# Kernel optimization log

Hardware: AMD Instinct MI355X
Metric: run time of the kernel (lower is better)

The kernel has to match this reference:

```python
import jax, jax.numpy as jnp
import numpy as np

B, L, D, C, H, NB = 2, 2048, 256, 8, 8, 2
S = 2                        # spatial coord dim of s
E = 2 * D - (C + 1)          # id-embedding width per D*2-(C+1)
FIN = 1 + S + E + C          # z + s + id-embed + conditionals
MAXLOC = 4096
DH = (2 * D) // H            # per-head dim


def _ln(x, sc, b):
    m = x.mean(-1, keepdims=True)
    v = ((x - m) ** 2).mean(-1, keepdims=True)
    return (x - m) * jax.lax.rsqrt(v + 1e-6) * sc + b


def setup_inputs() -> dict:
    key = jax.random.key(0)
    ks = iter(jax.random.split(key, 64))
    nrm = lambda shape: jax.random.normal(next(ks), shape, jnp.float32) * 0.02
    inp = {
        "z": jax.random.normal(next(ks), (B, L), jnp.float32),
        "conditionals": jax.random.normal(next(ks), (C,), jnp.float32),
        "s": jax.random.uniform(next(ks), (L, S), jnp.float32),
        "K": jax.random.uniform(next(ks), (L, L), jnp.float32),
        "embed": nrm((MAXLOC, E)),
        "W_in1": nrm((FIN, 4 * D)), "b_in1": jnp.zeros((4 * D,), jnp.float32),
        "W_in2": nrm((4 * D, D)), "b_in2": jnp.zeros((D,), jnp.float32),
        "bias_w": jnp.ones((NB,), jnp.float32), "bias_b": jnp.zeros((NB,), jnp.float32),
        "Wq": nrm((NB, D, 2 * D)), "bq": jnp.zeros((NB, 2 * D), jnp.float32),
        "Wk": nrm((NB, D, 2 * D)), "bk": jnp.zeros((NB, 2 * D), jnp.float32),
        "Wv": nrm((NB, D, 2 * D)), "bv": jnp.zeros((NB, 2 * D), jnp.float32),
        "Wo": nrm((NB, 2 * D, D)), "bo": jnp.zeros((NB, D), jnp.float32),
        "ln1_s": jnp.ones((NB, D), jnp.float32), "ln1_b": jnp.zeros((NB, D), jnp.float32),
        "ln2_s": jnp.ones((NB, D), jnp.float32), "ln2_b": jnp.zeros((NB, D), jnp.float32),
        "Wf1": nrm((NB, D, 4 * D)), "bf1": jnp.zeros((NB, 4 * D), jnp.float32),
        "Wf2": nrm((NB, 4 * D, D)), "bf2": jnp.zeros((NB, D), jnp.float32),
        "Wh1": nrm((D, 128)), "bh1": jnp.zeros((128,), jnp.float32),
        "Wh2": nrm((128, 1)), "bh2": jnp.zeros((1,), jnp.float32),
    }
    return inp


def reference(z, conditionals, s, K, embed, W_in1, b_in1, W_in2, b_in2,
              bias_w, bias_b, Wq, bq, Wk, bk, Wv, bv, Wo, bo,
              ln1_s, ln1_b, ln2_s, ln2_b, Wf1, bf1, Wf2, bf2,
              Wh1, bh1, Wh2, bh2):
    Bx, Lx = z.shape
    ids_e = embed[:Lx]  # ids = arange(L), so embedding lookup is a leading slice
    feats = jnp.concatenate([
        z[..., None],                                          # (B, L, 1)
        jnp.broadcast_to(s[None], (Bx, Lx, S)),                # (B, L, S)
        jnp.broadcast_to(ids_e[None], (Bx, Lx, E)),            # (B, L, E)
        jnp.broadcast_to(conditionals[None, None], (Bx, Lx, C)),  # cond_as_feats
    ], axis=-1)
    x = jax.nn.gelu(feats @ W_in1 + b_in1) @ W_in2 + b_in2     # (B, L, D)
    for i in range(NB):
        bias = bias_w[i] * K + bias_b[i]                        # learned scalar-affine kernel bias (L, L)
        h = _ln(x, ln1_s[i], ln1_b[i])
        q = (h @ Wq[i] + bq[i]).reshape(Bx, Lx, H, DH)
        k = (h @ Wk[i] + bk[i]).reshape(Bx, Lx, H, DH)
        v = (h @ Wv[i] + bv[i]).reshape(Bx, Lx, H, DH)
        scores = jnp.einsum('bqhd,bkhd->bhqk', q, k) / jnp.sqrt(jnp.float32(DH))
        scores = scores + bias[None, None]                      # broadcast over batch, heads
        a = jax.nn.softmax(scores, axis=-1)
        o = jnp.einsum('bhqk,bkhd->bqhd', a, v).reshape(Bx, Lx, 2 * D)
        x = x + (o @ Wo[i] + bo[i])
        h2 = _ln(x, ln2_s[i], ln2_b[i])
        x = x + jax.nn.gelu(h2 @ Wf1[i] + bf1[i]) @ Wf2[i] + bf2[i]
    return jax.nn.gelu(x @ Wh1 + bh1) @ Wh2 + bh2              # head MLP([128,1]) -> (B, L, 1)
```

## Files before the change

### kernel.cpp

```cpp
#include <hip/hip_runtime.h>
#include <math.h>

#define B_SZ 2
#define L_LEN 2048
#define D_MOD 256
#define H_HEADS 8
#define NB_BLK 2
#define S_SZ 2
#define E_SZ 503
#define C_SZ 8
#define FIN 514
#define FIN_PAD 576
#define LOG2E 1.44269504088896340736f
#define QSC (0.125f * LOG2E)

typedef short bf16x8 __attribute__((ext_vector_type(8)));
typedef float f32x4 __attribute__((ext_vector_type(4)));
typedef unsigned short u16x4 __attribute__((ext_vector_type(4)));
typedef unsigned short u16x8 __attribute__((ext_vector_type(8)));

#define OFF_IN1 0
#define OFF_IN2 589824
#define OFF_QKV 851968
#define OFF_O   1638400
#define OFF_F1  1900544
#define OFF_F2  2424832
#define OFF_H   2949120
#define WT_END  3047424

__device__ __forceinline__ unsigned short f2bf(float x) {
    unsigned u = __float_as_uint(x);
    u += 0x7FFFu + ((u >> 16) & 1u);
    return (unsigned short)(u >> 16);
}

__device__ __forceinline__ float bf2f(unsigned short h) {
    return __uint_as_float(((unsigned)h) << 16);
}

__device__ __forceinline__ float gelu_f(float x) {
    float x3 = x * x * x;
    return 0.5f * x * (1.0f + tanhf(0.7978845608028654f * (x + 0.044715f * x3)));
}

__device__ __forceinline__ void gll16(const void* g, void* l) {
    __builtin_amdgcn_global_load_lds(
        (const __attribute__((address_space(1))) unsigned int*)g,
        (__attribute__((address_space(3))) unsigned int*)l,
        16, 0, 0);
}

__global__ __launch_bounds__(256) void prep_kernel(
    const float* __restrict__ W_in1, const float* __restrict__ W_in2,
    const float* __restrict__ Wq, const float* __restrict__ Wk,
    const float* __restrict__ Wv, const float* __restrict__ Wo,
    const float* __restrict__ Wf1, const float* __restrict__ Wf2,
    const float* __restrict__ Wh1, const float* __restrict__ Kmat,
    const float* __restrict__ bias_w,
    const float* __restrict__ bq, const float* __restrict__ bk,
    const float* __restrict__ bv,
    const float* __restrict__ z, const float* __restrict__ s,
    const float* __restrict__ embed, const float* __restrict__ cond,
    unsigned short* __restrict__ wt, unsigned short* __restrict__ kmfrag,
    float* __restrict__ bqkv, unsigned short* __restrict__ feats)
{
    __shared__ unsigned short sT[64][65];
    int b = blockIdx.x;
    int t = threadIdx.x;

    if (b < 720) {
        const float* src; unsigned short* dst; int K, N, Kp, tile;
        float scale = 1.0f;
        if (b < 144)      { src = W_in1; dst = wt + OFF_IN1; K = 514;  N = 1024; Kp = 576;  tile = b; }
        else if (b < 208) { src = W_in2; dst = wt + OFF_IN2; K = 1024; N = 256;  Kp = 1024; tile = b - 144; }
        else if (b < 400) { int t2 = b - 208;
                            int sec = t2 >> 5; tile = t2 & 31;
                            int i = sec / 3, which = sec % 3;
                            const float* wsrc = which == 0 ? Wq : which == 1 ? Wk : Wv;
                            if (which == 0) scale = QSC;
                            src = wsrc + (size_t)i * 131072;
                            dst = wt + OFF_QKV + (size_t)i * 393216 + (size_t)which * 131072;
                            K = 256; N = 512; Kp = 256; }
        else if (b < 464) { int t2 = b - 400; int i = t2 >> 5; tile = t2 & 31;
                            src = Wo + (size_t)i * 131072; dst = wt + OFF_O + (size_t)i * 131072;
                            K = 512; N = 256; Kp = 512; }
        else if (b < 592) { int t2 = b - 464; int i = t2 >> 6; tile = t2 & 63;
                            src = Wf1 + (size_t)i * 262144; dst = wt + OFF_F1 + (size_t)i * 262144;
                            K = 256; N = 1024; Kp = 256; }
        else              { int t2 = b - 592; int i = t2 >> 6; tile = t2 & 63;
                            src = Wf2 + (size_t)i * 262144; dst = wt + OFF_F2 + (size_t)i * 262144;
                            K = 1024; N = 256; Kp = 1024; }

        int nt = N >> 6;
        int kt0 = (tile / nt) << 6;
        int nt0 = (tile % nt) << 6;
        #pragma unroll
        for (int p = 0; p < 4; p++) {
            int r = p * 16 + (t >> 4);
            int c = (t & 15) * 4;
            float4 v4 = make_float4(0.f, 0.f, 0.f, 0.f);
            if (kt0 + r < K) v4 = *(const float4*)(src + (size_t)(kt0 + r) * N + nt0 + c);
            sT[r][c + 0] = f2bf(v4.x * scale);
            sT[r][c + 1] = f2bf(v4.y * scale);
            sT[r][c + 2] = f2bf(v4.z * scale);
            sT[r][c + 3] = f2bf(v4.w * scale);
        }
        __syncthreads();
        int n = t >> 2, kq = (t & 3) * 16;
        u16x8 o0, o1;
        #pragma unroll
        for (int j = 0; j < 8; j++) {
            o0[j] = sT[kq + j][n];
            o1[j] = sT[kq + 8 + j][n];
        }
        unsigned short* dp = dst + (size_t)(nt0 + n) * Kp + kt0 + kq;
        *(u16x8*)(dp) = o0;
        *(u16x8*)(dp + 8) = o1;
    } else if (b < 1104) {
        int idx = (b - 720) * 256 + t;
        if (idx < 128 * 768) {
            int n = idx / 768, kk = idx % 768;
            int kz = kk & 255;
            float v = Wh1[(size_t)kz * 128 + n];
            unsigned short hi = f2bf(v);
            wt[OFF_H + idx] = (kk < 512) ? hi : f2bf(v - bf2f(hi));
        }
    } else if (b < 3152) {
        int t2 = b - 1104;
        int i = t2 >> 10, rem = t2 & 1023;
        int kt = rem >> 5, qb = rem & 31;
        float sc = bias_w[i] * LOG2E;
        int q0 = qb * 64 + ((t >> 6) << 4) + (((t >> 4) & 3) << 2);
        int k0 = kt * 64 + (t & 15);
        u16x8 f0, f1;
        #pragma unroll
        for (int c = 0; c < 4; c++)
            #pragma unroll
            for (int r = 0; r < 4; r++) {
                float v = Kmat[(size_t)(q0 + r) * L_LEN + k0 + c * 16] * sc;
                if (c < 2) f0[c * 4 + r] = f2bf(v);
                else       f1[(c - 2) * 4 + r] = f2bf(v);
            }
        unsigned short* dp = kmfrag + ((size_t)i << 22)
                           + (((size_t)(kt * 32 + qb)) * 256 + t) * 16;
        *(u16x8*)dp = f0;
        *(u16x8*)(dp + 8) = f1;
    } else if (b < 3164) {
        int idx = (b - 3152) * 256 + t;
        if (idx < 2 * 1536) {
            int i = idx / 1536, c = idx % 1536;
            float v;
            if (c < 512)       v = bq[i * 512 + c] * QSC;
            else if (c < 1024) v = bk[i * 512 + c - 512];
            else               v = bv[i * 512 + c - 1024];
            bqkv[idx] = v;
        }
    } else {
        int idx = (b - 3164) * 256 + t;
        const int total = B_SZ * L_LEN * FIN_PAD;
        if (idx < total) {
            int f = idx % FIN_PAD;
            int row = idx / FIN_PAD;
            int l = row % L_LEN;
            float val;
            if (f == 0)                   val = z[row];
            else if (f < 1 + S_SZ)        val = s[l * S_SZ + (f - 1)];
            else if (f < 1 + S_SZ + E_SZ) val = embed[(size_t)l * E_SZ + (f - 3)];
            else if (f < FIN)             val = cond[f - (1 + S_SZ + E_SZ)];
            else                          val = 0.0f;
            feats[idx] = f2bf(val);
        }
    }
}

template<int ACT, int OMODE>
__global__ __launch_bounds__(256) void gemmW(
    const unsigned short* __restrict__ A, const unsigned short* __restrict__ Wt,
    const float* __restrict__ bias, unsigned short* __restrict__ Cb,
    unsigned short* __restrict__ Cbk, unsigned short* __restrict__ Cbv,
    int M, int N, int Kd, int lda)
{
    __shared__ unsigned short sA[2][64][64];
    __shared__ unsigned short sB[2][128][64];
    const int tid = threadIdx.x;
    const int l = tid & 63, w = tid >> 6;
    const int g = l >> 4, n16 = l & 15;
    const int wr = w >> 1, wc = w & 1;
    const int m0 = blockIdx.y * 64, n0 = blockIdx.x * 128;
    const int r8 = l >> 3;
    const int swz8 = ((l & 7) ^ r8) * 8;

    f32x4 acc[2][4];
    #pragma unroll
    for (int mi = 0; mi < 2; mi++)
        #pragma unroll
        for (int ni = 0; ni < 4; ni++)
            acc[mi][ni] = (f32x4){0.f, 0.f, 0.f, 0.f};

#define STAGEW(buf, k0)                                                         \
    do {                                                                        \
        _Pragma("unroll")                                                       \
        for (int p = 0; p < 2; p++) {                                           \
            int row = w * 16 + p * 8 + r8;                                      \
            gll16(A + (size_t)(m0 + row) * lda + (k0) + swz8,                   \
                  &sA[buf][w * 16 + p * 8][0]);                                 \
        }                                                                       \
        _Pragma("unroll")                                                       \
        for (int p = 0; p < 4; p++) {                                           \
            int row = w * 32 + p * 8 + r8;                                      \
            gll16(Wt + (size_t)(n0 + row) * Kd + (k0) + swz8,                   \
                  &sB[buf][w * 32 + p * 8][0]);                                 \
        }                                                                       \
    } while (0)

    STAGEW(0, 0);
    __syncthreads();

    int cur = 0;
    for (int k0 = 0; k0 < Kd; k0 += 64) {
        int nxt = cur ^ 1;
        if (k0 + 64 < Kd) STAGEW(nxt, k0 + 64);
        #pragma unroll
        for (int ks = 0; ks < 2; ks++) {
            bf16x8 af[2], bfr[4];
            #pragma unroll
            for (int mi = 0; mi < 2; mi++) {
                int row = wr * 32 + mi * 16 + n16;
                af[mi] = *(const bf16x8*)((const char*)&sA[cur][row][0]
                          + ((ks * 64 + g * 16) ^ ((n16 & 7) << 4)));
            }
            #pragma unroll
            for (int ni = 0; ni < 4; ni++) {
                int row = wc * 64 + ni * 16 + n16;
                bfr[ni] = *(const bf16x8*)((const char*)&sB[cur][row][0]
                          + ((ks * 64 + g * 16) ^ ((n16 & 7) << 4)));
            }
            #pragma unroll
            for (int mi = 0; mi < 2; mi++)
                #pragma unroll
                for (int ni = 0; ni < 4; ni++)
                    acc[mi][ni] = __builtin_amdgcn_mfma_f32_16x16x32_bf16(
                        af[mi], bfr[ni], acc[mi][ni], 0, 0, 0);
        }
        __syncthreads();
        cur = nxt;
    }
#undef STAGEW

    #pragma unroll
    for (int mi = 0; mi < 2; mi++) {
        #pragma unroll
        for (int ni = 0; ni < 4; ni++) {
            int col = n0 + wc * 64 + ni * 16 + n16;
            float bv = bias[col];
            #pragma unroll
            for (int r = 0; r < 4; r++) {
                int row = m0 + wr * 32 + mi * 16 + 4 * g + r;
                float val = acc[mi][ni][r] + bv;
                if (ACT == 1) val = gelu_f(val);
                if (OMODE == 1) {
                    Cb[(size_t)row * N + col] = f2bf(val);
                } else {
                    if (col < 1024) {
                        unsigned short* dst = (col < 512) ? Cb : Cbk;
                        dst[(size_t)row * 512 + (col & 511)] = f2bf(val);
                    } else {
                        Cbv[((size_t)(row >> 11) * 512 + (col - 1024)) * L_LEN + (row & (L_LEN - 1))] = f2bf(val);
                    }
                }
            }
        }
    }
}

template<int ACT, int OMODE, int BM>
__global__ __launch_bounds__(256) void gemm_bf16(
    const unsigned short* __restrict__ A, const unsigned short* __restrict__ Wt,
    const float* __restrict__ bias, float* __restrict__ Cf,
    unsigned short* __restrict__ Cb, int M, int N, int Kd, int lda)
{
    __shared__ unsigned short sA[2][BM][64];
    __shared__ unsigned short sB[2][64][64];
    const int tid = threadIdx.x;
    const int l = tid & 63, w = tid >> 6;
    const int g = l >> 4, n16 = l & 15;
    const int m0 = blockIdx.y * BM, n0 = blockIdx.x * 64;

    const int r8 = l >> 3;
    const int swz8 = ((l & 7) ^ r8) * 8;

    const int NMI = (BM == 64) ? 2 : 1;
    const int wr = w >> 1;
    const int wc = w & 1;

    f32x4 acc[2][2];
    #pragma unroll
    for (int mi = 0; mi < 2; mi++)
        #pragma unroll
        for (int ni = 0; ni < 2; ni++)
            acc[mi][ni] = (f32x4){0.f, 0.f, 0.f, 0.f};

#define STAGE(buf, k0)                                                          \
    do {                                                                        \
        if (BM == 64) {                                                         \
            _Pragma("unroll")                                                   \
            for (int p = 0; p < 2; p++) {                                       \
                int row = w * 16 + p * 8 + r8;                                  \
                gll16(A + (size_t)(m0 + row) * lda + (k0) + swz8,               \
                      &sA[buf][w * 16 + p * 8][0]);                             \
            }                                                                   \
        } else {                                                                \
            int row = w * 8 + r8;                                               \
            gll16(A + (size_t)(m0 + row) * lda + (k0) + swz8,                   \
                  &sA[buf][w * 8][0]);                                          \
        }                                                                       \
        _Pragma("unroll")                                                       \
        for (int p = 0; p < 2; p++) {                                           \
            int row = w * 16 + p * 8 + r8;                                      \
            gll16(Wt + (size_t)(n0 + row) * Kd + (k0) + swz8,                   \
                  &sB[buf][w * 16 + p * 8][0]);                                 \
        }                                                                       \
    } while (0)

    STAGE(0, 0);
    __syncthreads();

    int cur = 0;
    for (int k0 = 0; k0 < Kd; k0 += 64) {
        int nxt = cur ^ 1;
        if (k0 + 64 < Kd) STAGE(nxt, k0 + 64);
        #pragma unroll
        for (int ks = 0; ks < 2; ks++) {
            bf16x8 af[2], bfr[2];
            #pragma unroll
            for (int mi = 0; mi < NMI; mi++) {
                int row = (BM == 64) ? (wr * 32 + mi * 16 + n16) : (wr * 16 + n16);
                af[mi] = *(const bf16x8*)((const char*)&sA[cur][row][0]
                          + ((ks * 64 + g * 16) ^ ((n16 & 7) << 4)));
            }
            #pragma unroll
            for (int ni = 0; ni < 2; ni++) {
                int row = wc * 32 + ni * 16 + n16;
                bfr[ni] = *(const bf16x8*)((const char*)&sB[cur][row][0]
                          + ((ks * 64 + g * 16) ^ ((n16 & 7) << 4)));
            }
            #pragma unroll
            for (int mi = 0; mi < NMI; mi++)
                #pragma unroll
                for (int ni = 0; ni < 2; ni++)
                    acc[mi][ni] = __builtin_amdgcn_mfma_f32_16x16x32_bf16(
                        af[mi], bfr[ni], acc[mi][ni], 0, 0, 0);
        }
        __syncthreads();
        cur = nxt;
    }
#undef STAGE

    #pragma unroll
    for (int mi = 0; mi < NMI; mi++) {
        #pragma unroll
        for (int ni = 0; ni < 2; ni++) {
            int col = n0 + wc * 32 + ni * 16 + n16;
            float bv = bias[col];
            #pragma unroll
            for (int r = 0; r < 4; r++) {
                int row = (BM == 64) ? (m0 + wr * 32 + mi * 16 + 4 * g + r)
                                     : (m0 + wr * 16 + 4 * g + r);
                float val = acc[mi][ni][r] + bv;
                if (ACT == 1) val = gelu_f(val);
                if (OMODE == 0) {
                    Cf[(size_t)row * N + col] = val;
                } else if (OMODE == 1) {
                    Cb[(size_t)row * N + col] = f2bf(val);
                } else if (OMODE == 2) {
                    float* cp = Cf + (size_t)row * N + col;
                    *cp += val;
                } else if (OMODE == 5) {
                    float xnew = Cf[(size_t)row * N + col] + val;
                    unsigned short hi = f2bf(xnew);
                    unsigned short lo = f2bf(xnew - bf2f(hi));
                    unsigned short* orow = Cb + (size_t)row * 768;
                    orow[col] = hi;
                    orow[256 + col] = lo;
                    orow[512 + col] = hi;
                }
            }
        }
    }
}

__global__ __launch_bounds__(256) void ln_bf16(
    const float* __restrict__ x, const float* __restrict__ sc,
    const float* __restrict__ bi, unsigned short* __restrict__ out)
{
    int wave = threadIdx.x >> 6, lane = threadIdx.x & 63;
    int row = blockIdx.x * 4 + wave;
    const float* xr = x + (size_t)row * D_MOD;
    float4 v = *(const float4*)(xr + lane * 4);
    float s1 = v.x + v.y + v.z + v.w;
    float s2 = v.x * v.x + v.y * v.y + v.z * v.z + v.w * v.w;
    #pragma unroll
    for (int off = 1; off < 64; off <<= 1) {
        s1 += __shfl_xor(s1, off);
        s2 += __shfl_xor(s2, off);
    }
    float mean = s1 * (1.0f / 256.0f);
    float var = s2 * (1.0f / 256.0f) - mean * mean;
    float rs = rsqrtf(var + 1e-6f);
    float4 scv = *(const float4*)(sc + lane * 4);
    float4 bv  = *(const float4*)(bi + lane * 4);
    u16x4 o4;
    o4[0] = f2bf((v.x - mean) * rs * scv.x + bv.x);
    o4[1] = f2bf((v.y - mean) * rs * scv.y + bv.y);
    o4[2] = f2bf((v.z - mean) * rs * scv.z + bv.z);
    o4[3] = f2bf((v.w - mean) * rs * scv.w + bv.w);
    *(u16x4*)(out + (size_t)row * D_MOD + lane * 4) = o4;
}

__global__ __launch_bounds__(256, 2) void attn_mfma(
    const unsigned short* __restrict__ q, const unsigned short* __restrict__ k,
    const unsigned short* __restrict__ vt, const unsigned short* __restrict__ kmf,
    unsigned short* __restrict__ o)
{
    __shared__ unsigned short sK[2][64][64];
    __shared__ unsigned short sV[2][64][64];
    __shared__ unsigned short sP[4][16][72];

    const int tid = threadIdx.x;
    const int l = tid & 63, w = tid >> 6;
    const int g = l >> 4, n16 = l & 15;
    const int qblk = blockIdx.x * 64, hh = blockIdx.y, b = blockIdx.z;

    const int r8 = l >> 3;
    const int swz8 = ((l & 7) ^ r8) * 8;

    bf16x8 qf[2];
    {
        const unsigned short* qp = q + (size_t)(b * L_LEN + qblk + w * 16 + n16) * 512 + hh * 64;
        qf[0] = *(const bf16x8*)(qp + g * 8);
        qf[1] = *(const bf16x8*)(qp + 32 + g * 8);
    }
    bf16x8 onesf;
    #pragma unroll
    for (int j = 0; j < 8; j++) onesf[j] = (short)0x3F80;

    f32x4 o_acc[4];
    #pragma unroll
    for (int c = 0; c < 4; c++) o_acc[c] = (f32x4){0.f, 0.f, 0.f, 0.f};
    f32x4 l_acc = (f32x4){0.f, 0.f, 0.f, 0.f};

    const unsigned short* kbase = k + (size_t)b * L_LEN * 512 + hh * 64;
    const unsigned short* vbase = vt + ((size_t)b * 512 + hh * 64) * L_LEN;
    const unsigned short* kmbase = kmf + ((size_t)blockIdx.x * 256 + tid) * 16;

    #pragma unroll
    for (int p = 0; p < 2; p++) {
        int row = w * 16 + p * 8 + r8;
        gll16(kbase + (size_t)row * 512 + swz8, &sK[0][w * 16 + p * 8][0]);
        gll16(vbase + (size_t)row * L_LEN + swz8, &sV[0][w * 16 + p * 8][0]);
    }
    u16x8 kmC0 = *(const u16x8*)kmbase;
    u16x8 kmC1 = *(const u16x8*)(kmbase + 8);
    __syncthreads();

    int cur = 0;
    for (int kt = 0; kt < L_LEN / 64; kt++) {
        const int nb = cur ^ 1;
        const int kblk2 = (kt + 1) << 6;
        u16x8 kmN0 = kmC0, kmN1 = kmC1;
        if (kt + 1 < L_LEN / 64) {
            #pragma unroll
            for (int p = 0; p < 2; p++) {
                int row = w * 16 + p * 8 + r8;
                gll16(kbase + (size_t)(kblk2 + row) * 512 + swz8, &sK[nb][w * 16 + p * 8][0]);
                gll16(vbase + (size_t)row * L_LEN + kblk2 + swz8, &sV[nb][w * 16 + p * 8][0]);
            }
            const unsigned short* kp2 = kmbase + (size_t)(kt + 1) * 131072;
            kmN0 = *(const u16x8*)kp2;
            kmN1 = *(const u16x8*)(kp2 + 8);
        }
        f32x4 sacc[4];
        #pragma unroll
        for (int c = 0; c < 4; c++)
            #pragma unroll
            for (int r = 0; r < 4; r++)
                sacc[c][r] = bf2f((unsigned short)(c < 2 ? kmC0[c * 4 + r] : kmC1[(c - 2) * 4 + r]));
        __builtin_amdgcn_s_setprio(1);
        #pragma unroll
        for (int ks = 0; ks < 2; ks++)
            #pragma unroll
            for (int c = 0; c < 4; c++) {
                int row = c * 16 + n16;
                bf16x8 kf = *(const bf16x8*)((const char*)&sK[cur][row][0]
                             + ((ks * 64 + g * 16) ^ ((n16 & 7) << 4)));
                sacc[c] = __builtin_amdgcn_mfma_f32_16x16x32_bf16(qf[ks], kf, sacc[c], 0, 0, 0);
            }
        __builtin_amdgcn_s_setprio(0);
        float p[4][4];
        #pragma unroll
        for (int r = 0; r < 4; r++)
            #pragma unroll
            for (int c = 0; c < 4; c++)
                p[r][c] = __builtin_amdgcn_exp2f(sacc[c][r]);
        #pragma unroll
        for (int r = 0; r < 4; r++)
            #pragma unroll
            for (int c = 0; c < 4; c++)
                sP[w][4 * g + r][c * 16 + n16] = f2bf(p[r][c]);
        __builtin_amdgcn_s_setprio(1);
        #pragma unroll
        for (int ks = 0; ks < 2; ks++) {
            bf16x8 pf = *(const bf16x8*)&sP[w][n16][ks * 32 + g * 8];
            l_acc = __builtin_amdgcn_mfma_f32_16x16x32_bf16(pf, onesf, l_acc, 0, 0, 0);
            #pragma unroll
            for (int c = 0; c < 4; c++) {
                int row = c * 16 + n16;
                bf16x8 vf = *(const bf16x8*)((const char*)&sV[cur][row][0]
                             + ((ks * 64 + g * 16) ^ ((n16 & 7) << 4)));
                o_acc[c] = __builtin_amdgcn_mfma_f32_16x16x32_bf16(pf, vf, o_acc[c], 0, 0, 0);
            }
        }
        __builtin_amdgcn_s_setprio(0);
        __syncthreads();
        cur = nb;
        kmC0 = kmN0;
        kmC1 = kmN1;
    }

    float inv[4];
    #pragma unroll
    for (int r = 0; r < 4; r++) inv[r] = 1.0f / l_acc[r];
    #pragma unroll
    for (int c = 0; c < 4; c++)
        #pragma unroll
        for (int r = 0; r < 4; r++)
            o[(size_t)(b * L_LEN + qblk + w * 16 + 4 * g + r) * 512 + hh * 64 + c * 16 + n16]
                = f2bf(o_acc[c][r] * inv[r]);
}

__global__ __launch_bounds__(256) void hsum_kernel(
    const unsigned short* __restrict__ hb, const float* __restrict__ Wh2,
    const float* __restrict__ bh2, float* __restrict__ out)
{
    int wave = threadIdx.x >> 6, lane = threadIdx.x & 63;
    int row = blockIdx.x * 4 + wave;
    unsigned v = *(const unsigned*)(hb + (size_t)row * 128 + lane * 2);
    float v0 = __uint_as_float((v & 0xFFFFu) << 16);
    float v1 = __uint_as_float(v & 0xFFFF0000u);
    float val = v0 * Wh2[lane * 2] + v1 * Wh2[lane * 2 + 1];
    #pragma unroll
    for (int off = 1; off < 64; off <<= 1)
        val += __shfl_xor(val, off);
    if (lane == 0) out[row] = val + bh2[0];
}

extern "C" void kernel_launch(void* const* d_in, const int* in_sizes, int n_in,
                              void* d_out, int out_size, void* d_ws, size_t ws_size,
                              hipStream_t stream)
{
    const float* z      = (const float*)d_in[0];
    const float* cond   = (const float*)d_in[1];
    const float* s      = (const float*)d_in[2];
    const float* Kmat   = (const float*)d_in[3];
    const float* embed  = (const float*)d_in[4];
    const float* W_in1  = (const float*)d_in[5];
    const float* b_in1  = (const float*)d_in[6];
    const float* W_in2  = (const float*)d_in[7];
    const float* b_in2  = (const float*)d_in[8];
    const float* bias_w = (const float*)d_in[9];
    const float* bias_b = (const float*)d_in[10];
    const float* Wq     = (const float*)d_in[11];
    const float* bq     = (const float*)d_in[12];
    const float* Wk     = (const float*)d_in[13];
    const float* bk     = (const float*)d_in[14];
    const float* Wv     = (const float*)d_in[15];
    const float* bv     = (const float*)d_in[16];
    const float* Wo     = (const float*)d_in[17];
    const float* bo     = (const float*)d_in[18];
    const float* ln1_s  = (const float*)d_in[19];
    const float* ln1_b  = (const float*)d_in[20];
    const float* ln2_s  = (const float*)d_in[21];
    const float* ln2_b  = (const float*)d_in[22];
    const float* Wf1    = (const float*)d_in[23];
    const float* bf1    = (const float*)d_in[24];
    const float* Wf2    = (const float*)d_in[25];
    const float* bf2    = (const float*)d_in[26];
    const float* Wh1    = (const float*)d_in[27];
    const float* bh1    = (const float*)d_in[28];
    const float* Wh2    = (const float*)d_in[29];
    const float* bh2    = (const float*)d_in[30];
    float* out = (float*)d_out;
    (void)bias_b;

    const int M = B_SZ * L_LEN;
    char* base = (char*)d_ws;
    unsigned short* feats = (unsigned short*)base;
    float* x = (float*)(base + (size_t)M * FIN_PAD * 2);
    unsigned short* h    = (unsigned short*)((char*)x + (size_t)M * D_MOD * 4);
    unsigned short* hid1 = h    + (size_t)M * D_MOD;
    unsigned short* qb   = hid1 + (size_t)M * 1024;
    unsigned short* kb2  = qb   + (size_t)M * 512;
    unsigned short* vtb  = kb2  + (size_t)M * 512;
    unsigned short* ob   = vtb  + (size_t)M * 512;
    unsigned short* wt   = ob   + (size_t)M * 512;
    float* bqkv          = (float*)(wt + WT_END);
    unsigned short* kmfrag = (unsigned short*)(bqkv + 2 * 1536);

    prep_kernel<<<dim3(12380), dim3(256), 0, stream>>>(
        W_in1, W_in2, Wq, Wk, Wv, Wo, Wf1, Wf2, Wh1, Kmat, bias_w,
        bq, bk, bv, z, s, embed, cond, wt, kmfrag, bqkv, feats);

    gemmW<1, 1><<<dim3(8, 64), 256, 0, stream>>>(feats, wt + OFF_IN1, b_in1, hid1, nullptr, nullptr, M, 1024, FIN_PAD, FIN_PAD);
    gemm_bf16<0, 0, 32><<<dim3(4, 128), 256, 0, stream>>>(hid1, wt + OFF_IN2, b_in2, x, nullptr, M, 256, 1024, 1024);

    for (int i = 0; i < NB_BLK; i++) {
        ln_bf16<<<dim3(M / 4), 256, 0, stream>>>(x, ln1_s + i * D_MOD, ln1_b + i * D_MOD, h);
        gemmW<0, 4><<<dim3(12, 64), 256, 0, stream>>>(h, wt + OFF_QKV + (size_t)i * 393216, bqkv + i * 1536, qb, kb2, vtb, M, 1536, 256, 256);
        attn_mfma<<<dim3(L_LEN / 64, H_HEADS, B_SZ), 256, 0, stream>>>(qb, kb2, vtb, kmfrag + ((size_t)i << 22), ob);
        gemm_bf16<0, 2, 32><<<dim3(4, 128), 256, 0, stream>>>(ob, wt + OFF_O + (size_t)i * 131072, bo + i * D_MOD, x, nullptr, M, 256, 512, 512);
        ln_bf16<<<dim3(M / 4), 256, 0, stream>>>(x, ln2_s + i * D_MOD, ln2_b + i * D_MOD, h);
        gemmW<1, 1><<<dim3(8, 64), 256, 0, stream>>>(h, wt + OFF_F1 + (size_t)i * 262144, bf1 + i * 1024, hid1, nullptr, nullptr, M, 1024, 256, 256);
        if (i == 0)
            gemm_bf16<0, 2, 32><<<dim3(4, 128), 256, 0, stream>>>(hid1, wt + OFF_F2 + (size_t)i * 262144, bf2 + i * D_MOD, x, nullptr, M, 256, 1024, 1024);
        else
            gemm_bf16<0, 5, 32><<<dim3(4, 128), 256, 0, stream>>>(hid1, wt + OFF_F2 + (size_t)i * 262144, bf2 + i * D_MOD, x, qb, M, 256, 1024, 1024);
    }
    gemm_bf16<1, 1, 64><<<dim3(2, 64), 256, 0, stream>>>(qb, wt + OFF_H, bh1, nullptr, ob, M, 128, 768, 768);
    hsum_kernel<<<dim3(M / 4), 256, 0, stream>>>(ob, Wh2, bh2, out);
}
```

Baseline: 240.3 us.

## Add BM=16 GEMM tile variant and batch prep work per thread

Adds a 16-row tile mode to gemm_bf16, in which each of the four waves computes a 16x16 output strip, and switches the N=256/128 projections to it with twice as many blocks. The goal is to fill more compute units on these small GEMMs. The cost is less reuse of the weight tile per block. The prep kernel also computes both blocks' scaled bias fragments from one read of K, and writes feature rows four elements at a time for both batches, which cuts the prep grid from 12380 to 3292 blocks.

```diff
diff --git a/kernel.cpp b/kernel.cpp
--- a/kernel.cpp
+++ b/kernel.cpp
@@ -125,28 +125,29 @@
             unsigned short hi = f2bf(v);
             wt[OFF_H + idx] = (kk < 512) ? hi : f2bf(v - bf2f(hi));
         }
-    } else if (b < 3152) {
-        int t2 = b - 1104;
-        int i = t2 >> 10, rem = t2 & 1023;
-        int kt = rem >> 5, qb = rem & 31;
-        float sc = bias_w[i] * LOG2E;
+    } else if (b < 2128) {
+        int tile = b - 1104;
+        int kt = tile >> 5, qb = tile & 31;
+        float s0 = bias_w[0] * LOG2E, s1 = bias_w[1] * LOG2E;
         int q0 = qb * 64 + ((t >> 6) << 4) + (((t >> 4) & 3) << 2);
         int k0 = kt * 64 + (t & 15);
-        u16x8 f0, f1;
+        u16x8 a0, a1, b0, b1;
         #pragma unroll
         for (int c = 0; c < 4; c++)
             #pragma unroll
             for (int r = 0; r < 4; r++) {
-                float v = Kmat[(size_t)(q0 + r) * L_LEN + k0 + c * 16] * sc;
-                if (c < 2) f0[c * 4 + r] = f2bf(v);
-                else       f1[(c - 2) * 4 + r] = f2bf(v);
-            }
-        unsigned short* dp = kmfrag + ((size_t)i << 22)
-                           + (((size_t)(kt * 32 + qb)) * 256 + t) * 16;
-        *(u16x8*)dp = f0;
-        *(u16x8*)(dp + 8) = f1;
-    } else if (b < 3164) {
-        int idx = (b - 3152) * 256 + t;
+                float v = Kmat[(size_t)(q0 + r) * L_LEN + k0 + c * 16];
+                if (c < 2) { a0[c * 4 + r] = f2bf(v * s0); b0[c * 4 + r] = f2bf(v * s1); }
+                else       { a1[(c - 2) * 4 + r] = f2bf(v * s0); b1[(c - 2) * 4 + r] = f2bf(v * s1); }
+            }
+        unsigned short* dp = kmfrag + (((size_t)(kt * 32 + qb)) * 256 + t) * 16;
+        *(u16x8*)dp = a0;
+        *(u16x8*)(dp + 8) = a1;
+        unsigned short* dp1 = dp + ((size_t)1 << 22);
+        *(u16x8*)dp1 = b0;
+        *(u16x8*)(dp1 + 8) = b1;
+    } else if (b < 2140) {
+        int idx = (b - 2128) * 256 + t;
         if (idx < 2 * 1536) {
             int i = idx / 1536, c = idx % 1536;
             float v;
@@ -156,20 +157,24 @@
             bqkv[idx] = v;
         }
     } else {
-        int idx = (b - 3164) * 256 + t;
-        const int total = B_SZ * L_LEN * FIN_PAD;
-        if (idx < total) {
-            int f = idx % FIN_PAD;
-            int row = idx / FIN_PAD;
-            int l = row % L_LEN;
+        int idx = (b - 2140) * 256 + t;
+        int l = idx / 144;
+        int f0 = (idx % 144) * 4;
+        u16x4 pk0, pk1;
+        #pragma unroll
+        for (int j = 0; j < 4; j++) {
+            int f = f0 + j;
             float val;
-            if (f == 0)                   val = z[row];
-            else if (f < 1 + S_SZ)        val = s[l * S_SZ + (f - 1)];
-            else if (f < 1 + S_SZ + E_SZ) val = embed[(size_t)l * E_SZ + (f - 3)];
-            else if (f < FIN)             val = cond[f - (1 + S_SZ + E_SZ)];
-            else                          val = 0.0f;
-            feats[idx] = f2bf(val);
-        }
+            if (f >= 3 && f < 506)      val = embed[(size_t)l * E_SZ + (f - 3)];
+            else if (f >= 1 && f < 3)   val = s[l * S_SZ + (f - 1)];
+            else if (f >= 506 && f < FIN) val = cond[f - 506];
+            else                        val = 0.0f;
+            unsigned short hv = f2bf(val);
+            pk0[j] = (f == 0) ? f2bf(z[l]) : hv;
+            pk1[j] = (f == 0) ? f2bf(z[L_LEN + l]) : hv;
+        }
+        *(u16x4*)(feats + (size_t)l * FIN_PAD + f0) = pk0;
+        *(u16x4*)(feats + (size_t)(L_LEN + l) * FIN_PAD + f0) = pk1;
     }
 }
 
@@ -290,6 +295,7 @@
     const int swz8 = ((l & 7) ^ r8) * 8;
 
     const int NMI = (BM == 64) ? 2 : 1;
+    const int NNI = (BM == 16) ? 1 : 2;
     const int wr = w >> 1;
     const int wc = w & 1;
 
@@ -309,10 +315,16 @@
                 gll16(A + (size_t)(m0 + row) * lda + (k0) + swz8,               \
                       &sA[buf][w * 16 + p * 8][0]);                             \
             }                                                                   \
-        } else {                                                                \
+        } else if (BM == 32) {                                                  \
             int row = w * 8 + r8;                                               \
             gll16(A + (size_t)(m0 + row) * lda + (k0) + swz8,                   \
                   &sA[buf][w * 8][0]);                                          \
+        } else {                                                                \
+            if (w < 2) {                                                        \
+                int row = w * 8 + r8;                                           \
+                gll16(A + (size_t)(m0 + row) * lda + (k0) + swz8,               \
+                      &sA[buf][w * 8][0]);                                      \
+            }                                                                   \
         }                                                                       \
         _Pragma("unroll")                                                       \
         for (int p = 0; p < 2; p++) {                                           \
@@ -334,20 +346,21 @@
             bf16x8 af[2], bfr[2];
             #pragma unroll
             for (int mi = 0; mi < NMI; mi++) {
-                int row = (BM == 64) ? (wr * 32 + mi * 16 + n16) : (wr * 16 + n16);
+                int row = (BM == 64) ? (wr * 32 + mi * 16 + n16)
+                        : (BM == 32) ? (wr * 16 + n16) : n16;
                 af[mi] = *(const bf16x8*)((const char*)&sA[cur][row][0]
                           + ((ks * 64 + g * 16) ^ ((n16 & 7) << 4)));
             }
             #pragma unroll
-            for (int ni = 0; ni < 2; ni++) {
-                int row = wc * 32 + ni * 16 + n16;
+            for (int ni = 0; ni < NNI; ni++) {
+                int row = (BM == 16) ? (w * 16 + n16) : (wc * 32 + ni * 16 + n16);
                 bfr[ni] = *(const bf16x8*)((const char*)&sB[cur][row][0]
                           + ((ks * 64 + g * 16) ^ ((n16 & 7) << 4)));
             }
             #pragma unroll
             for (int mi = 0; mi < NMI; mi++)
                 #pragma unroll
-                for (int ni = 0; ni < 2; ni++)
+                for (int ni = 0; ni < NNI; ni++)
                     acc[mi][ni] = __builtin_amdgcn_mfma_f32_16x16x32_bf16(
                         af[mi], bfr[ni], acc[mi][ni], 0, 0, 0);
         }
@@ -359,13 +372,15 @@
     #pragma unroll
     for (int mi = 0; mi < NMI; mi++) {
         #pragma unroll
-        for (int ni = 0; ni < 2; ni++) {
-            int col = n0 + wc * 32 + ni * 16 + n16;
+        for (int ni = 0; ni < NNI; ni++) {
+            int col = (BM == 16) ? (n0 + w * 16 + n16)
+                                 : (n0 + wc * 32 + ni * 16 + n16);
             float bv = bias[col];
             #pragma unroll
             for (int r = 0; r < 4; r++) {
                 int row = (BM == 64) ? (m0 + wr * 32 + mi * 16 + 4 * g + r)
-                                     : (m0 + wr * 16 + 4 * g + r);
+                        : (BM == 32) ? (m0 + wr * 16 + 4 * g + r)
+                                     : (m0 + 4 * g + r);
                 float val = acc[mi][ni][r] + bv;
                 if (ACT == 1) val = gelu_f(val);
                 if (OMODE == 0) {
@@ -606,25 +621,25 @@
     float* bqkv          = (float*)(wt + WT_END);
     unsigned short* kmfrag = (unsigned short*)(bqkv + 2 * 1536);
 
-    prep_kernel<<<dim3(12380), dim3(256), 0, stream>>>(
+    prep_kernel<<<dim3(3292), dim3(256), 0, stream>>>(
         W_in1, W_in2, Wq, Wk, Wv, Wo, Wf1, Wf2, Wh1, Kmat, bias_w,
         bq, bk, bv, z, s, embed, cond, wt, kmfrag, bqkv, feats);
 
     gemmW<1, 1><<<dim3(8, 64), 256, 0, stream>>>(feats, wt + OFF_IN1, b_in1, hid1, nullptr, nullptr, M, 1024, FIN_PAD, FIN_PAD);
-    gemm_bf16<0, 0, 32><<<dim3(4, 128), 256, 0, stream>>>(hid1, wt + OFF_IN2, b_in2, x, nullptr, M, 256, 1024, 1024);
+    gemm_bf16<0, 0, 16><<<dim3(4, 256), 256, 0, stream>>>(hid1, wt + OFF_IN2, b_in2, x, nullptr, M, 256, 1024, 1024);
 
     for (int i = 0; i < NB_BLK; i++) {
         ln_bf16<<<dim3(M / 4), 256, 0, stream>>>(x, ln1_s + i * D_MOD, ln1_b + i * D_MOD, h);
         gemmW<0, 4><<<dim3(12, 64), 256, 0, stream>>>(h, wt + OFF_QKV + (size_t)i * 393216, bqkv + i * 1536, qb, kb2, vtb, M, 1536, 256, 256);
         attn_mfma<<<dim3(L_LEN / 64, H_HEADS, B_SZ), 256, 0, stream>>>(qb, kb2, vtb, kmfrag + ((size_t)i << 22), ob);
-        gemm_bf16<0, 2, 32><<<dim3(4, 128), 256, 0, stream>>>(ob, wt + OFF_O + (size_t)i * 131072, bo + i * D_MOD, x, nullptr, M, 256, 512, 512);
+        gemm_bf16<0, 2, 16><<<dim3(4, 256), 256, 0, stream>>>(ob, wt + OFF_O + (size_t)i * 131072, bo + i * D_MOD, x, nullptr, M, 256, 512, 512);
         ln_bf16<<<dim3(M / 4), 256, 0, stream>>>(x, ln2_s + i * D_MOD, ln2_b + i * D_MOD, h);
         gemmW<1, 1><<<dim3(8, 64), 256, 0, stream>>>(h, wt + OFF_F1 + (size_t)i * 262144, bf1 + i * 1024, hid1, nullptr, nullptr, M, 1024, 256, 256);
         if (i == 0)
-            gemm_bf16<0, 2, 32><<<dim3(4, 128), 256, 0, stream>>>(hid1, wt + OFF_F2 + (size_t)i * 262144, bf2 + i * D_MOD, x, nullptr, M, 256, 1024, 1024);
+            gemm_bf16<0, 2, 16><<<dim3(4, 256), 256, 0, stream>>>(hid1, wt + OFF_F2 + (size_t)i * 262144, bf2 + i * D_MOD, x, nullptr, M, 256, 1024, 1024);
         else
-            gemm_bf16<0, 5, 32><<<dim3(4, 128), 256, 0, stream>>>(hid1, wt + OFF_F2 + (size_t)i * 262144, bf2 + i * D_MOD, x, qb, M, 256, 1024, 1024);
-    }
-    gemm_bf16<1, 1, 64><<<dim3(2, 64), 256, 0, stream>>>(qb, wt + OFF_H, bh1, nullptr, ob, M, 128, 768, 768);
+            gemm_bf16<0, 5, 16><<<dim3(4, 256), 256, 0, stream>>>(hid1, wt + OFF_F2 + (size_t)i * 262144, bf2 + i * D_MOD, x, qb, M, 256, 1024, 1024);
+    }
+    gemm_bf16<1, 1, 16><<<dim3(2, 256), 256, 0, stream>>>(qb, wt + OFF_H, bh1, nullptr, ob, M, 128, 768, 768);
     hsum_kernel<<<dim3(M / 4), 256, 0, stream>>>(ob, Wh2, bh2, out);
 }
```

New measurement: 232.8 us. 3.1% less time.
